# Performance work log

Hardware: AMD Instinct MI355X
Metric: run time of the kernel (lower is better)

## Reference

```python
import jax, jax.numpy as jnp
import numpy as np

C, G = 128, 2000          # num_cells, total_genes
CE, GE, H = 64, 64, 256   # cell_embed_dim, gene_embed_dim, hidden_dim
F = CE + GE + 3           # FCGNN input: ctrl val + cell_embed + gene_embed + shift + num_cells


def setup_inputs() -> dict:
    key = jax.random.key(0)
    ks = jax.random.split(key, 13)
    s = 0.02
    return {
        "ctrl": jax.random.uniform(ks[0], (C, G), dtype=jnp.float32),
        "shift_vec": jax.random.normal(ks[1], (G,), dtype=jnp.float32),
        "gene_indices": jnp.arange(G, dtype=jnp.int32),
        # CellEmbedding params
        "ce_w1": jax.random.normal(ks[2], (G, H), dtype=jnp.float32) * s,
        "ce_b1": jnp.zeros((H,), dtype=jnp.float32),
        "ce_w2": jax.random.normal(ks[3], (H, CE), dtype=jnp.float32) * s,
        "ce_b2": jnp.zeros((CE,), dtype=jnp.float32),
        # gene embedding table
        "gene_table": jax.random.normal(ks[4], (G, GE), dtype=jnp.float32) * s,
        # FCGNN params
        "g_w1": jax.random.normal(ks[5], (F, H), dtype=jnp.float32) * s,
        "g_b1": jnp.zeros((H,), dtype=jnp.float32),
        "g_w2": jax.random.normal(ks[6], (2 * H, H), dtype=jnp.float32) * s,
        "g_b2": jnp.zeros((H,), dtype=jnp.float32),
        "g_w3": jax.random.normal(ks[7], (2 * H, 1), dtype=jnp.float32) * s,
        "g_b3": jnp.zeros((1,), dtype=jnp.float32),
    }


def reference(ctrl, shift_vec, gene_indices, ce_w1, ce_b1, ce_w2, ce_b2,
              gene_table, g_w1, g_b1, g_w2, g_b2, g_w3, g_b3):
    num_cells = ctrl.shape[0]
    num_genes = gene_indices.shape[0]

    # CellEmbedding: fc2(elu(fc1(ctrl)))  -> [C, CE]
    ce = jax.nn.elu(ctrl @ ce_w1 + ce_b1) @ ce_w2 + ce_b2

    ctrl_g = ctrl[:, gene_indices]           # [C, Gn]
    shift = shift_vec[gene_indices]          # [Gn]
    ge = gene_table[gene_indices]            # [Gn, GE]

    # Build [C, Gn, F] feature tensor (ctrl val, cell embed, gene embed, shift, num_cells)
    z = jnp.concatenate([
        ctrl_g[:, :, None],
        jnp.broadcast_to(ce[:, None, :], (num_cells, num_genes, ce.shape[1])),
        jnp.broadcast_to(ge[None, :, :], (num_cells, num_genes, ge.shape[1])),
        jnp.broadcast_to(shift[None, :, None], (num_cells, num_genes, 1)),
        jnp.full((num_cells, num_genes, 1), float(num_cells), dtype=ctrl.dtype),
    ], axis=2)

    # FCGNN applied per gene (vectorized over gene axis); pooling is mean over cells (axis 0)
    x = jax.nn.elu(z @ g_w1 + g_b1)                                   # [C, Gn, H]
    p = x.mean(axis=0)                                                # [Gn, H]
    x = jnp.concatenate([x, jnp.broadcast_to(p[None], x.shape)], -1) @ g_w2 + g_b2
    p = x.mean(axis=0)
    x = jax.nn.elu(jnp.concatenate([x, jnp.broadcast_to(p[None], x.shape)], -1)) @ g_w3 + g_b3
    out = x[..., 0]                                                   # [C, Gn]

    # softmax over cells (torch Softmax(dim=0) after transpose/squeeze)
    return jax.nn.softmax(out, axis=0)
```

## Files before the change

### kernel.cpp

```cpp
#include <hip/hip_runtime.h>
#include <math.h>

#define G_GENES 2000
#define C_CELLS 128
#define H_DIM   256
#define CE_DIM  64
#define LDAe    260

typedef __attribute__((ext_vector_type(8))) short short8;
typedef __attribute__((ext_vector_type(4))) float floatx4;

__device__ __forceinline__ float eluf(float x) {
    float e = __expf(x) - 1.0f;
    return x > 0.0f ? x : e;
}
__device__ __forceinline__ unsigned short f2bf(float v) {
    unsigned u = __float_as_uint(v);
    u += 0x7FFF + ((u >> 16) & 1);
    return (unsigned short)(u >> 16);
}

__global__ __launch_bounds__(1024) void k_prep(
    const float* __restrict__ ctrl, const float* __restrict__ ce_w1,
    const float* __restrict__ ce_b1, const float* __restrict__ ce_w2,
    const float* __restrict__ ce_b2, const float* __restrict__ g_w1,
    const float* __restrict__ g_b1, const float* __restrict__ shiftv,
    const int* __restrict__ gidx, const float* __restrict__ gtab,
    const float* __restrict__ g_w2,
    float* __restrict__ Atc, unsigned short* __restrict__ w2abt,
    float* __restrict__ Bvg)
{
    const int b = blockIdx.x;
    const int t = threadIdx.x;

    if (b < C_CELLS) {
        __shared__ float crow[G_GENES];
        __shared__ float hidp[4][H_DIM];
        __shared__ float hid[H_DIM];
        __shared__ float celp[16 * CE_DIM];
        __shared__ float cel[CE_DIM];
        const int c = b;
        for (int i = t; i < G_GENES; i += 1024) crow[i] = ctrl[(size_t)c * G_GENES + i];
        __syncthreads();

        {
            const int h = t & 255, kq = t >> 8;
            float s[10];
            #pragma unroll
            for (int j = 0; j < 10; ++j) s[j] = 0.f;
            const float* w = ce_w1 + (size_t)(kq * 500) * H_DIM + h;
            const float* cr = crow + kq * 500;
            for (int k0 = 0; k0 < 50; ++k0) {
                #pragma unroll
                for (int j = 0; j < 10; ++j)
                    s[j] = fmaf(cr[k0 * 10 + j], w[(size_t)(k0 * 10 + j) * H_DIM], s[j]);
            }
            float ss = 0.f;
            #pragma unroll
            for (int j = 0; j < 10; ++j) ss += s[j];
            hidp[kq][h] = ss;
        }
        __syncthreads();
        if (t < H_DIM)
            hid[t] = eluf(hidp[0][t] + hidp[1][t] + hidp[2][t] + hidp[3][t] + ce_b1[t]);
        __syncthreads();

        {
            const int e = t & 63, grp = t >> 6;
            float cp = 0.f;
            #pragma unroll
            for (int hh = 0; hh < 16; ++hh)
                cp = fmaf(hid[grp * 16 + hh], ce_w2[(size_t)(grp * 16 + hh) * CE_DIM + e], cp);
            celp[grp * CE_DIM + e] = cp;
        }
        __syncthreads();
        if (t < CE_DIM) {
            float s = ce_b2[t];
            #pragma unroll
            for (int grp = 0; grp < 16; ++grp) s += celp[grp * CE_DIM + t];
            cel[t] = s;
        }
        __syncthreads();
        if (t < H_DIM) {
            float a = 0.f;
            #pragma unroll 8
            for (int e = 0; e < CE_DIM; ++e) a = fmaf(cel[e], g_w1[(size_t)(1 + e) * H_DIM + t], a);
            Atc[(size_t)c * H_DIM + t] = a;
        }
    } else if (b < C_CELLS + 8) {
        const int n  = (b - C_CELLS) * 32 + (t >> 5);
        const int k0 = (t & 31) * 8;
        unsigned v[8];
        #pragma unroll
        for (int j = 0; j < 8; ++j) v[j] = f2bf(g_w2[(size_t)(k0 + j) * H_DIM + n]);
        uint4 pk;
        pk.x = v[0] | (v[1] << 16);
        pk.y = v[2] | (v[3] << 16);
        pk.z = v[4] | (v[5] << 16);
        pk.w = v[6] | (v[7] << 16);
        *(uint4*)&w2abt[(size_t)n * H_DIM + k0] = pk;
    } else {
        const int g = (b - C_CELLS - 8) * 4 + (t >> 8);
        const int h = t & 255;
        const int idx = gidx[g];
        float bv = g_b1[h] + 128.0f * g_w1[(size_t)130 * H_DIM + h]
                 + shiftv[idx] * g_w1[(size_t)129 * H_DIM + h];
        #pragma unroll 8
        for (int e = 0; e < CE_DIM; ++e)
            bv = fmaf(gtab[(size_t)idx * CE_DIM + e], g_w1[(size_t)(65 + e) * H_DIM + h], bv);
        Bvg[(size_t)g * H_DIM + h] = bv;
    }
}

__global__ __launch_bounds__(512, 4) void k_main(
    const float* __restrict__ ctrl, const int* __restrict__ gidx,
    const float* __restrict__ g_w1, const float* __restrict__ g_w2,
    const float* __restrict__ g_b2, const float* __restrict__ g_w3,
    const float* __restrict__ Atc, const float* __restrict__ Bvg,
    const unsigned short* __restrict__ w2abt, float* __restrict__ out)
{
    __shared__ __align__(16) unsigned short x1t[C_CELLS * LDAe];
    __shared__ __align__(16) float scratch[8 * LDAe];
    __shared__ __align__(16) float Bvl[H_DIM];
    __shared__ __align__(16) float w1l[H_DIM];
    __shared__ float qv[H_DIM];
    __shared__ float w3v[H_DIM];
    __shared__ float cc[C_CELLS];
    __shared__ float wred[4];

    const int g = blockIdx.x;
    const int t = threadIdx.x;
    const int idx = gidx[g];

    const int lane = t & 63;
    const int w    = t >> 6;
    const int quad = lane >> 4;
    const int nlo  = lane & 15;
    const int wm   = w >> 2;
    const int wn   = w & 3;

    const unsigned short* bbase = w2abt + (size_t)(wn * 64 + nlo) * H_DIM + quad * 8;
    short8 bcur[4];
    #pragma unroll
    for (int nt = 0; nt < 4; ++nt)
        bcur[nt] = *(const short8*)(bbase + (size_t)nt * 16 * H_DIM);

    if (t < C_CELLS) cc[t] = ctrl[(size_t)t * G_GENES + idx];
    if (t < H_DIM) {
        Bvl[t] = Bvg[(size_t)g * H_DIM + t];
        w1l[t] = g_w1[t];
        w3v[t] = g_w3[t];
    }
    __syncthreads();

    {
        const int ho = t & 31, cgrp = t >> 5;
        const int h0 = ho * 8;
        float4 wv0 = *(const float4*)(w1l + h0);
        float4 wv1 = *(const float4*)(w1l + h0 + 4);
        float4 bv0 = *(const float4*)(Bvl + h0);
        float4 bv1 = *(const float4*)(Bvl + h0 + 4);
        float s[8];
        #pragma unroll
        for (int j = 0; j < 8; ++j) s[j] = 0.f;
        #pragma unroll
        for (int i = 0; i < 8; ++i) {
            const int c = cgrp * 8 + i;
            const float ccv = cc[c];
            float4 a0 = *(const float4*)(Atc + (size_t)c * H_DIM + h0);
            float4 a1 = *(const float4*)(Atc + (size_t)c * H_DIM + h0 + 4);
            float v0 = eluf(fmaf(ccv, wv0.x, a0.x + bv0.x));
            float v1 = eluf(fmaf(ccv, wv0.y, a0.y + bv0.y));
            float v2 = eluf(fmaf(ccv, wv0.z, a0.z + bv0.z));
            float v3 = eluf(fmaf(ccv, wv0.w, a0.w + bv0.w));
            float v4 = eluf(fmaf(ccv, wv1.x, a1.x + bv1.x));
            float v5 = eluf(fmaf(ccv, wv1.y, a1.y + bv1.y));
            float v6 = eluf(fmaf(ccv, wv1.z, a1.z + bv1.z));
            float v7 = eluf(fmaf(ccv, wv1.w, a1.w + bv1.w));
            s[0] += v0; s[1] += v1; s[2] += v2; s[3] += v3;
            s[4] += v4; s[5] += v5; s[6] += v6; s[7] += v7;
            uint4 pk;
            pk.x = (unsigned)f2bf(v0) | ((unsigned)f2bf(v1) << 16);
            pk.y = (unsigned)f2bf(v2) | ((unsigned)f2bf(v3) << 16);
            pk.z = (unsigned)f2bf(v4) | ((unsigned)f2bf(v5) << 16);
            pk.w = (unsigned)f2bf(v6) | ((unsigned)f2bf(v7) << 16);
            *(uint4*)&x1t[c * LDAe + h0] = pk;
        }
        #pragma unroll
        for (int j = 0; j < 8; ++j) s[j] += __shfl_xor(s[j], 32);
        if (lane < 32) {
            float4 p0 = {s[0], s[1], s[2], s[3]};
            float4 p1 = {s[4], s[5], s[6], s[7]};
            *(float4*)&scratch[w * LDAe + h0] = p0;
            *(float4*)&scratch[w * LDAe + h0 + 4] = p1;
        }
    }
    __syncthreads();

    floatx4 acc[4][4];
    #pragma unroll
    for (int mt = 0; mt < 4; ++mt)
        #pragma unroll
        for (int nt = 0; nt < 4; ++nt)
            acc[mt][nt] = (floatx4){0.f, 0.f, 0.f, 0.f};

    const unsigned short* abase = &x1t[(wm * 64 + nlo) * LDAe + quad * 8];

    #pragma unroll
    for (int kt = 0; kt < 8; ++kt) {
        short8 af[4];
        #pragma unroll
        for (int mt = 0; mt < 4; ++mt)
            af[mt] = *(const short8*)(abase + mt * 16 * LDAe + kt * 32);
        short8 bnx[4];
        if (kt < 7) {
            #pragma unroll
            for (int nt = 0; nt < 4; ++nt)
                bnx[nt] = *(const short8*)(bbase + (size_t)nt * 16 * H_DIM + (kt + 1) * 32);
        }
        #pragma unroll
        for (int nt = 0; nt < 4; ++nt)
            #pragma unroll
            for (int mt = 0; mt < 4; ++mt)
                acc[mt][nt] = __builtin_amdgcn_mfma_f32_16x16x32_bf16(af[mt], bcur[nt], acc[mt][nt], 0, 0, 0);
        if (kt < 7) {
            #pragma unroll
            for (int nt = 0; nt < 4; ++nt) bcur[nt] = bnx[nt];
        }
    }

    if (t < H_DIM) {
        float ps = 0.f;
        #pragma unroll
        for (int w2 = 0; w2 < 8; ++w2) ps += scratch[w2 * LDAe + t];
        w1l[t] = ps * (1.0f / 128.0f);
    }
    __syncthreads();

    {
        const int j = t & 255, hf = t >> 8;
        float qp = 0.f;
        const float* w2b = g_w2 + (size_t)(H_DIM + hf * 128) * H_DIM + j;
        const float* pv = w1l + hf * 128;
        #pragma unroll 16
        for (int h = 0; h < 128; ++h) qp = fmaf(pv[h], w2b[(size_t)h * H_DIM], qp);
        if (hf) Bvl[j] = qp;
        __syncthreads();
        if (!hf) qv[j] = qp + Bvl[j] + g_b2[j];
    }
    __syncthreads();

    float* red2 = scratch;
    float qj[4], w3j[4];
    #pragma unroll
    for (int nt = 0; nt < 4; ++nt) {
        const int j = wn * 64 + nt * 16 + nlo;
        qj[nt] = qv[j];
        w3j[nt] = w3v[j];
    }
    #pragma unroll
    for (int mt = 0; mt < 4; ++mt) {
        #pragma unroll
        for (int reg = 0; reg < 4; ++reg) {
            float part = 0.f;
            #pragma unroll
            for (int nt = 0; nt < 4; ++nt)
                part = fmaf(eluf(acc[mt][nt][reg] + qj[nt]), w3j[nt], part);
            part += __shfl_xor(part, 1);
            part += __shfl_xor(part, 2);
            part += __shfl_xor(part, 4);
            part += __shfl_xor(part, 8);
            if (nlo == 0)
                red2[(wm * 64 + mt * 16 + quad * 4 + reg) * 5 + wn] = part;
        }
    }
    __syncthreads();

    float s = 0.f, e = 0.f;
    if (t < C_CELLS) {
        s = red2[t * 5 + 0] + red2[t * 5 + 1] + red2[t * 5 + 2] + red2[t * 5 + 3];
        float m = s;
        #pragma unroll
        for (int off = 1; off < 64; off <<= 1) m = fmaxf(m, __shfl_xor(m, off));
        if (lane == 0) wred[w] = m;
    }
    __syncthreads();
    if (t < C_CELLS) {
        const float m = fmaxf(wred[0], wred[1]);
        e = __expf(s - m);
        float S = e;
        #pragma unroll
        for (int off = 1; off < 64; off <<= 1) S += __shfl_xor(S, off);
        if (lane == 0) wred[2 + w] = S;
    }
    __syncthreads();
    if (t < C_CELLS) out[(size_t)t * G_GENES + g] = e / (wred[2] + wred[3]);
}

extern "C" void kernel_launch(void* const* d_in, const int* in_sizes, int n_in,
                              void* d_out, int out_size, void* d_ws, size_t ws_size,
                              hipStream_t stream) {
    const float* ctrl   = (const float*)d_in[0];
    const float* shiftv = (const float*)d_in[1];
    const int*   gidx   = (const int*)d_in[2];
    const float* ce_w1  = (const float*)d_in[3];
    const float* ce_b1  = (const float*)d_in[4];
    const float* ce_w2  = (const float*)d_in[5];
    const float* ce_b2  = (const float*)d_in[6];
    const float* gtab   = (const float*)d_in[7];
    const float* g_w1   = (const float*)d_in[8];
    const float* g_b1   = (const float*)d_in[9];
    const float* g_w2   = (const float*)d_in[10];
    const float* g_b2   = (const float*)d_in[11];
    const float* g_w3   = (const float*)d_in[12];

    char* ws = (char*)d_ws;
    float* Atc            = (float*)(ws);
    unsigned short* w2abt = (unsigned short*)(ws + 128 * 1024);
    float* Bvg            = (float*)(ws + 256 * 1024);
    float* out            = (float*)d_out;

    k_prep<<<C_CELLS + 8 + G_GENES / 4, 1024, 0, stream>>>(
        ctrl, ce_w1, ce_b1, ce_w2, ce_b2, g_w1, g_b1, shiftv, gidx, gtab, g_w2,
        Atc, w2abt, Bvg);
    k_main<<<G_GENES, 512, 0, stream>>>(ctrl, gidx, g_w1, g_w2, g_b2, g_w3,
                                        Atc, Bvg, w2abt, out);
}
```

Measured before the change: 217.9 us.

## Hoist per-gene pooled-mean projection into a batched kernel; pair cells in prep

Adds a new kernel, k_pq, that computes the layer-1 mean over cells and its projection through the pooled half of g_w2 for 8 genes per block. Each g_w2 read is reused across genes instead of being re-read by every gene block. k_main then loads the precomputed q vector, which drops its fp32 sum reduction, the matvec and two barriers. The cell-embedding prep now handles two cells per block, so each ce_w1 load serves two rows. The trade-offs are an extra launch, layer-1 activations (ELU) being computed twice, and an intermediate q_all buffer written to and read back from global memory.

```diff
diff --git a/kernel.cpp b/kernel.cpp
--- a/kernel.cpp
+++ b/kernel.cpp
@@ -33,62 +33,75 @@
     const int b = blockIdx.x;
     const int t = threadIdx.x;
 
-    if (b < C_CELLS) {
-        __shared__ float crow[G_GENES];
-        __shared__ float hidp[4][H_DIM];
-        __shared__ float hid[H_DIM];
-        __shared__ float celp[16 * CE_DIM];
-        __shared__ float cel[CE_DIM];
-        const int c = b;
-        for (int i = t; i < G_GENES; i += 1024) crow[i] = ctrl[(size_t)c * G_GENES + i];
+    if (b < 64) {
+        __shared__ float crow[2][G_GENES];
+        __shared__ float hidp[4][2][H_DIM];
+        __shared__ float hid[2][H_DIM];
+        __shared__ float celp[16][2][CE_DIM];
+        __shared__ float cel[2][CE_DIM];
+        const int c0 = b * 2;
+        for (int i = t; i < G_GENES; i += 1024) {
+            crow[0][i] = ctrl[(size_t)c0 * G_GENES + i];
+            crow[1][i] = ctrl[(size_t)(c0 + 1) * G_GENES + i];
+        }
         __syncthreads();
 
         {
             const int h = t & 255, kq = t >> 8;
-            float s[10];
-            #pragma unroll
-            for (int j = 0; j < 10; ++j) s[j] = 0.f;
+            float a0 = 0.f, a1 = 0.f, b0 = 0.f, b1 = 0.f;
             const float* w = ce_w1 + (size_t)(kq * 500) * H_DIM + h;
-            const float* cr = crow + kq * 500;
-            for (int k0 = 0; k0 < 50; ++k0) {
-                #pragma unroll
-                for (int j = 0; j < 10; ++j)
-                    s[j] = fmaf(cr[k0 * 10 + j], w[(size_t)(k0 * 10 + j) * H_DIM], s[j]);
+            const float* r0 = crow[0] + kq * 500;
+            const float* r1 = crow[1] + kq * 500;
+            #pragma unroll 5
+            for (int k = 0; k < 500; k += 2) {
+                float w0 = w[(size_t)k * H_DIM];
+                float w1v = w[(size_t)(k + 1) * H_DIM];
+                a0 = fmaf(r0[k], w0, a0);     b0 = fmaf(r1[k], w0, b0);
+                a1 = fmaf(r0[k + 1], w1v, a1); b1 = fmaf(r1[k + 1], w1v, b1);
             }
-            float ss = 0.f;
-            #pragma unroll
-            for (int j = 0; j < 10; ++j) ss += s[j];
-            hidp[kq][h] = ss;
-        }
-        __syncthreads();
-        if (t < H_DIM)
-            hid[t] = eluf(hidp[0][t] + hidp[1][t] + hidp[2][t] + hidp[3][t] + ce_b1[t]);
+            hidp[kq][0][h] = a0 + a1;
+            hidp[kq][1][h] = b0 + b1;
+        }
+        __syncthreads();
+        if (t < 512) {
+            const int cc_ = t >> 8, h = t & 255;
+            hid[cc_][h] = eluf(hidp[0][cc_][h] + hidp[1][cc_][h] + hidp[2][cc_][h]
+                             + hidp[3][cc_][h] + ce_b1[h]);
+        }
         __syncthreads();
 
         {
             const int e = t & 63, grp = t >> 6;
-            float cp = 0.f;
-            #pragma unroll
-            for (int hh = 0; hh < 16; ++hh)
-                cp = fmaf(hid[grp * 16 + hh], ce_w2[(size_t)(grp * 16 + hh) * CE_DIM + e], cp);
-            celp[grp * CE_DIM + e] = cp;
-        }
-        __syncthreads();
-        if (t < CE_DIM) {
-            float s = ce_b2[t];
-            #pragma unroll
-            for (int grp = 0; grp < 16; ++grp) s += celp[grp * CE_DIM + t];
-            cel[t] = s;
-        }
-        __syncthreads();
-        if (t < H_DIM) {
+            float c0p = 0.f, c1p = 0.f;
+            #pragma unroll
+            for (int hh = 0; hh < 16; ++hh) {
+                const int h = grp * 16 + hh;
+                float wv = ce_w2[(size_t)h * CE_DIM + e];
+                c0p = fmaf(hid[0][h], wv, c0p);
+                c1p = fmaf(hid[1][h], wv, c1p);
+            }
+            celp[grp][0][e] = c0p;
+            celp[grp][1][e] = c1p;
+        }
+        __syncthreads();
+        if (t < 128) {
+            const int cc_ = t >> 6, e = t & 63;
+            float s = ce_b2[e];
+            #pragma unroll
+            for (int grp = 0; grp < 16; ++grp) s += celp[grp][cc_][e];
+            cel[cc_][e] = s;
+        }
+        __syncthreads();
+        if (t < 512) {
+            const int cc_ = t >> 8, h = t & 255;
             float a = 0.f;
             #pragma unroll 8
-            for (int e = 0; e < CE_DIM; ++e) a = fmaf(cel[e], g_w1[(size_t)(1 + e) * H_DIM + t], a);
-            Atc[(size_t)c * H_DIM + t] = a;
-        }
-    } else if (b < C_CELLS + 8) {
-        const int n  = (b - C_CELLS) * 32 + (t >> 5);
+            for (int e = 0; e < CE_DIM; ++e)
+                a = fmaf(cel[cc_][e], g_w1[(size_t)(1 + e) * H_DIM + h], a);
+            Atc[(size_t)(c0 + cc_) * H_DIM + h] = a;
+        }
+    } else if (b < 72) {
+        const int n  = (b - 64) * 32 + (t >> 5);
         const int k0 = (t & 31) * 8;
         unsigned v[8];
         #pragma unroll
@@ -100,7 +113,7 @@
         pk.w = v[6] | (v[7] << 16);
         *(uint4*)&w2abt[(size_t)n * H_DIM + k0] = pk;
     } else {
-        const int g = (b - C_CELLS - 8) * 4 + (t >> 8);
+        const int g = (b - 72) * 4 + (t >> 8);
         const int h = t & 255;
         const int idx = gidx[g];
         float bv = g_b1[h] + 128.0f * g_w1[(size_t)130 * H_DIM + h]
@@ -112,15 +125,83 @@
     }
 }
 
+__global__ __launch_bounds__(1024) void k_pq(
+    const float* __restrict__ ctrl, const int* __restrict__ gidx,
+    const float* __restrict__ g_w1, const float* __restrict__ g_w2,
+    const float* __restrict__ g_b2, const float* __restrict__ Atc,
+    const float* __restrict__ Bvg, float* __restrict__ q_all)
+{
+    __shared__ float ccl[C_CELLS][8];
+    __shared__ float pp[4][8][H_DIM];
+    __shared__ float pf[8][H_DIM];
+
+    const int g0 = blockIdx.x * 8;
+    const int t = threadIdx.x;
+
+    {
+        const int c = t >> 3, gg = t & 7;
+        if (t < 1024) ccl[c][gg] = ctrl[(size_t)c * G_GENES + gidx[g0 + gg]];
+    }
+    __syncthreads();
+
+    const int h = t & 255, cq = t >> 8;
+    {
+        const float w1h = g_w1[h];
+        float bv[8];
+        #pragma unroll
+        for (int gg = 0; gg < 8; ++gg) bv[gg] = Bvg[(size_t)(g0 + gg) * H_DIM + h];
+        float s[8];
+        #pragma unroll
+        for (int gg = 0; gg < 8; ++gg) s[gg] = 0.f;
+        for (int ci = 0; ci < 32; ++ci) {
+            const int c = cq * 32 + ci;
+            const float at = Atc[(size_t)c * H_DIM + h];
+            #pragma unroll
+            for (int gg = 0; gg < 8; ++gg)
+                s[gg] += eluf(fmaf(ccl[c][gg], w1h, at + bv[gg]));
+        }
+        #pragma unroll
+        for (int gg = 0; gg < 8; ++gg) pp[cq][gg][h] = s[gg];
+    }
+    __syncthreads();
+
+    {
+        const int i = t, gg = i >> 7, hh2 = (i & 127) * 2;
+        #pragma unroll
+        for (int u = 0; u < 2; ++u) {
+            const int hh = hh2 + u;
+            pf[gg][hh] = (pp[0][gg][hh] + pp[1][gg][hh] + pp[2][gg][hh] + pp[3][gg][hh])
+                         * (1.0f / 128.0f);
+        }
+    }
+    __syncthreads();
+
+    {
+        const int j = t & 255, gp = t >> 8;
+        float q0 = g_b2[j], q1 = g_b2[j];
+        const float* w2b = g_w2 + (size_t)H_DIM * H_DIM + j;
+        const float* p0 = pf[gp * 2];
+        const float* p1 = pf[gp * 2 + 1];
+        #pragma unroll 8
+        for (int hh = 0; hh < H_DIM; ++hh) {
+            const float wv = w2b[(size_t)hh * H_DIM];
+            q0 = fmaf(p0[hh], wv, q0);
+            q1 = fmaf(p1[hh], wv, q1);
+        }
+        q_all[(size_t)(g0 + gp * 2) * H_DIM + j] = q0;
+        q_all[(size_t)(g0 + gp * 2 + 1) * H_DIM + j] = q1;
+    }
+}
+
 __global__ __launch_bounds__(512, 4) void k_main(
     const float* __restrict__ ctrl, const int* __restrict__ gidx,
-    const float* __restrict__ g_w1, const float* __restrict__ g_w2,
-    const float* __restrict__ g_b2, const float* __restrict__ g_w3,
+    const float* __restrict__ g_w1, const float* __restrict__ g_w3,
     const float* __restrict__ Atc, const float* __restrict__ Bvg,
-    const unsigned short* __restrict__ w2abt, float* __restrict__ out)
+    const float* __restrict__ q_all, const unsigned short* __restrict__ w2abt,
+    float* __restrict__ out)
 {
     __shared__ __align__(16) unsigned short x1t[C_CELLS * LDAe];
-    __shared__ __align__(16) float scratch[8 * LDAe];
+    __shared__ float red2[C_CELLS * 5];
     __shared__ __align__(16) float Bvl[H_DIM];
     __shared__ __align__(16) float w1l[H_DIM];
     __shared__ float qv[H_DIM];
@@ -149,6 +230,7 @@
     if (t < H_DIM) {
         Bvl[t] = Bvg[(size_t)g * H_DIM + t];
         w1l[t] = g_w1[t];
+        qv[t]  = q_all[(size_t)g * H_DIM + t];
         w3v[t] = g_w3[t];
     }
     __syncthreads();
@@ -160,9 +242,6 @@
         float4 wv1 = *(const float4*)(w1l + h0 + 4);
         float4 bv0 = *(const float4*)(Bvl + h0);
         float4 bv1 = *(const float4*)(Bvl + h0 + 4);
-        float s[8];
-        #pragma unroll
-        for (int j = 0; j < 8; ++j) s[j] = 0.f;
         #pragma unroll
         for (int i = 0; i < 8; ++i) {
             const int c = cgrp * 8 + i;
@@ -177,8 +256,6 @@
             float v5 = eluf(fmaf(ccv, wv1.y, a1.y + bv1.y));
             float v6 = eluf(fmaf(ccv, wv1.z, a1.z + bv1.z));
             float v7 = eluf(fmaf(ccv, wv1.w, a1.w + bv1.w));
-            s[0] += v0; s[1] += v1; s[2] += v2; s[3] += v3;
-            s[4] += v4; s[5] += v5; s[6] += v6; s[7] += v7;
             uint4 pk;
             pk.x = (unsigned)f2bf(v0) | ((unsigned)f2bf(v1) << 16);
             pk.y = (unsigned)f2bf(v2) | ((unsigned)f2bf(v3) << 16);
@@ -186,14 +263,6 @@
             pk.w = (unsigned)f2bf(v6) | ((unsigned)f2bf(v7) << 16);
             *(uint4*)&x1t[c * LDAe + h0] = pk;
         }
-        #pragma unroll
-        for (int j = 0; j < 8; ++j) s[j] += __shfl_xor(s[j], 32);
-        if (lane < 32) {
-            float4 p0 = {s[0], s[1], s[2], s[3]};
-            float4 p1 = {s[4], s[5], s[6], s[7]};
-            *(float4*)&scratch[w * LDAe + h0] = p0;
-            *(float4*)&scratch[w * LDAe + h0 + 4] = p1;
-        }
     }
     __syncthreads();
 
@@ -229,28 +298,6 @@
         }
     }
 
-    if (t < H_DIM) {
-        float ps = 0.f;
-        #pragma unroll
-        for (int w2 = 0; w2 < 8; ++w2) ps += scratch[w2 * LDAe + t];
-        w1l[t] = ps * (1.0f / 128.0f);
-    }
-    __syncthreads();
-
-    {
-        const int j = t & 255, hf = t >> 8;
-        float qp = 0.f;
-        const float* w2b = g_w2 + (size_t)(H_DIM + hf * 128) * H_DIM + j;
-        const float* pv = w1l + hf * 128;
-        #pragma unroll 16
-        for (int h = 0; h < 128; ++h) qp = fmaf(pv[h], w2b[(size_t)h * H_DIM], qp);
-        if (hf) Bvl[j] = qp;
-        __syncthreads();
-        if (!hf) qv[j] = qp + Bvl[j] + g_b2[j];
-    }
-    __syncthreads();
-
-    float* red2 = scratch;
     float qj[4], w3j[4];
     #pragma unroll
     for (int nt = 0; nt < 4; ++nt) {
@@ -318,11 +365,12 @@
     float* Atc            = (float*)(ws);
     unsigned short* w2abt = (unsigned short*)(ws + 128 * 1024);
     float* Bvg            = (float*)(ws + 256 * 1024);
+    float* q_all          = (float*)(ws + 256 * 1024 + (size_t)G_GENES * H_DIM * 4);
     float* out            = (float*)d_out;
 
-    k_prep<<<C_CELLS + 8 + G_GENES / 4, 1024, 0, stream>>>(
+    k_prep<<<64 + 8 + G_GENES / 4, 1024, 0, stream>>>(
         ctrl, ce_w1, ce_b1, ce_w2, ce_b2, g_w1, g_b1, shiftv, gidx, gtab, g_w2,
         Atc, w2abt, Bvg);
-    k_main<<<G_GENES, 512, 0, stream>>>(ctrl, gidx, g_w1, g_w2, g_b2, g_w3,
-                                        Atc, Bvg, w2abt, out);
-}
+    k_pq<<<G_GENES / 8, 1024, 0, stream>>>(ctrl, gidx, g_w1, g_w2, g_b2, Atc, Bvg, q_all);
+    k_main<<<G_GENES, 512, 0, stream>>>(ctrl, gidx, g_w1, g_w3, Atc, Bvg, q_all, w2abt, out);
+}
```

New measurement: 238.7 us. 9.6% more time.

## Split-K the cell embedding matmul across many blocks and precompute bf16 transposed w2 halves

Applied to the files above, without the earlier changes.

The cell embedding fc1 is restructured from 128 big blocks into 1024 split-K blocks that write partial sums, followed by a small finishing kernel that reduces them and computes the rest of the embedding. The pooled-term matvec in the main kernel now reads a bf16 transposed copy of the second half of g_w2 instead of strided fp32 loads. Atc loads are hoisted ahead of the first barrier in the main kernel, and the bf16 packing now uses the library conversion. The split-K path adds an extra launch and a global partial-sum buffer. The bf16 weights reduce precision in the pooled term.

```diff
diff --git a/kernel.cpp b/kernel.cpp
--- a/kernel.cpp
+++ b/kernel.cpp
@@ -1,4 +1,5 @@
 #include <hip/hip_runtime.h>
+#include <hip/hip_bf16.h>
 #include <math.h>
 
 #define G_GENES 2000
@@ -14,93 +15,68 @@
     float e = __expf(x) - 1.0f;
     return x > 0.0f ? x : e;
 }
-__device__ __forceinline__ unsigned short f2bf(float v) {
-    unsigned u = __float_as_uint(v);
-    u += 0x7FFF + ((u >> 16) & 1);
-    return (unsigned short)(u >> 16);
-}
-
-__global__ __launch_bounds__(1024) void k_prep(
+__device__ __forceinline__ unsigned pk2(float a, float b) {
+    __hip_bfloat162 h2 = __float22bfloat162_rn(make_float2(a, b));
+    unsigned r; __builtin_memcpy(&r, &h2, 4); return r;
+}
+union U8 { unsigned u[4]; short8 s; uint4 v; };
+
+__global__ __launch_bounds__(512) void k_g1(
     const float* __restrict__ ctrl, const float* __restrict__ ce_w1,
-    const float* __restrict__ ce_b1, const float* __restrict__ ce_w2,
-    const float* __restrict__ ce_b2, const float* __restrict__ g_w1,
-    const float* __restrict__ g_b1, const float* __restrict__ shiftv,
-    const int* __restrict__ gidx, const float* __restrict__ gtab,
-    const float* __restrict__ g_w2,
-    float* __restrict__ Atc, unsigned short* __restrict__ w2abt,
-    float* __restrict__ Bvg)
+    const float* __restrict__ g_w1, const float* __restrict__ g_b1,
+    const float* __restrict__ shiftv, const int* __restrict__ gidx,
+    const float* __restrict__ gtab, const float* __restrict__ g_w2,
+    float* __restrict__ hidpart, unsigned short* __restrict__ w2abt,
+    unsigned short* __restrict__ w2bbt, float* __restrict__ Bvg)
 {
     const int b = blockIdx.x;
     const int t = threadIdx.x;
 
-    if (b < C_CELLS) {
-        __shared__ float crow[G_GENES];
-        __shared__ float hidp[4][H_DIM];
-        __shared__ float hid[H_DIM];
-        __shared__ float celp[16 * CE_DIM];
-        __shared__ float cel[CE_DIM];
-        const int c = b;
-        for (int i = t; i < G_GENES; i += 1024) crow[i] = ctrl[(size_t)c * G_GENES + i];
+    if (b < 1024) {
+        __shared__ float crow[2][128];
+        const int cpair = b >> 4;
+        const int kc    = b & 15;
+        const int csub  = t >> 8;
+        const int h     = t & 255;
+        const int c     = cpair * 2 + csub;
+
+        if (h < 125) crow[csub][h] = ctrl[(size_t)c * G_GENES + kc * 125 + h];
         __syncthreads();
 
-        {
-            const int h = t & 255, kq = t >> 8;
-            float s[10];
-            #pragma unroll
-            for (int j = 0; j < 10; ++j) s[j] = 0.f;
-            const float* w = ce_w1 + (size_t)(kq * 500) * H_DIM + h;
-            const float* cr = crow + kq * 500;
-            for (int k0 = 0; k0 < 50; ++k0) {
-                #pragma unroll
-                for (int j = 0; j < 10; ++j)
-                    s[j] = fmaf(cr[k0 * 10 + j], w[(size_t)(k0 * 10 + j) * H_DIM], s[j]);
-            }
-            float ss = 0.f;
-            #pragma unroll
-            for (int j = 0; j < 10; ++j) ss += s[j];
-            hidp[kq][h] = ss;
-        }
-        __syncthreads();
-        if (t < H_DIM)
-            hid[t] = eluf(hidp[0][t] + hidp[1][t] + hidp[2][t] + hidp[3][t] + ce_b1[t]);
-        __syncthreads();
-
-        {
-            const int e = t & 63, grp = t >> 6;
-            float cp = 0.f;
-            #pragma unroll
-            for (int hh = 0; hh < 16; ++hh)
-                cp = fmaf(hid[grp * 16 + hh], ce_w2[(size_t)(grp * 16 + hh) * CE_DIM + e], cp);
-            celp[grp * CE_DIM + e] = cp;
-        }
-        __syncthreads();
-        if (t < CE_DIM) {
-            float s = ce_b2[t];
-            #pragma unroll
-            for (int grp = 0; grp < 16; ++grp) s += celp[grp * CE_DIM + t];
-            cel[t] = s;
-        }
-        __syncthreads();
-        if (t < H_DIM) {
-            float a = 0.f;
-            #pragma unroll 8
-            for (int e = 0; e < CE_DIM; ++e) a = fmaf(cel[e], g_w1[(size_t)(1 + e) * H_DIM + t], a);
-            Atc[(size_t)c * H_DIM + t] = a;
-        }
-    } else if (b < C_CELLS + 8) {
-        const int n  = (b - C_CELLS) * 32 + (t >> 5);
+        float s0 = 0.f, s1 = 0.f, s2 = 0.f, s3 = 0.f, s4 = 0.f;
+        const float* w = ce_w1 + (size_t)(kc * 125) * H_DIM + h;
+        const float* cr = crow[csub];
+        #pragma unroll 5
+        for (int k = 0; k < 125; k += 5) {
+            s0 = fmaf(cr[k + 0], w[(size_t)(k + 0) * H_DIM], s0);
+            s1 = fmaf(cr[k + 1], w[(size_t)(k + 1) * H_DIM], s1);
+            s2 = fmaf(cr[k + 2], w[(size_t)(k + 2) * H_DIM], s2);
+            s3 = fmaf(cr[k + 3], w[(size_t)(k + 3) * H_DIM], s3);
+            s4 = fmaf(cr[k + 4], w[(size_t)(k + 4) * H_DIM], s4);
+        }
+        hidpart[((size_t)kc * C_CELLS + c) * H_DIM + h] = ((s0 + s1) + (s2 + s3)) + s4;
+    } else if (b < 1040) {
+        const int n  = (b - 1024) * 16 + (t >> 5);
         const int k0 = (t & 31) * 8;
-        unsigned v[8];
-        #pragma unroll
-        for (int j = 0; j < 8; ++j) v[j] = f2bf(g_w2[(size_t)(k0 + j) * H_DIM + n]);
-        uint4 pk;
-        pk.x = v[0] | (v[1] << 16);
-        pk.y = v[2] | (v[3] << 16);
-        pk.z = v[4] | (v[5] << 16);
-        pk.w = v[6] | (v[7] << 16);
-        *(uint4*)&w2abt[(size_t)n * H_DIM + k0] = pk;
+        float v[8];
+        #pragma unroll
+        for (int j = 0; j < 8; ++j) v[j] = g_w2[(size_t)(k0 + j) * H_DIM + n];
+        U8 u;
+        u.u[0] = pk2(v[0], v[1]); u.u[1] = pk2(v[2], v[3]);
+        u.u[2] = pk2(v[4], v[5]); u.u[3] = pk2(v[6], v[7]);
+        *(uint4*)&w2abt[(size_t)n * H_DIM + k0] = u.v;
+    } else if (b < 1056) {
+        const int j  = (b - 1040) * 16 + (t >> 5);
+        const int h0 = (t & 31) * 8;
+        float v[8];
+        #pragma unroll
+        for (int u2 = 0; u2 < 8; ++u2) v[u2] = g_w2[(size_t)(H_DIM + h0 + u2) * H_DIM + j];
+        U8 u;
+        u.u[0] = pk2(v[0], v[1]); u.u[1] = pk2(v[2], v[3]);
+        u.u[2] = pk2(v[4], v[5]); u.u[3] = pk2(v[6], v[7]);
+        *(uint4*)&w2bbt[(size_t)j * H_DIM + h0] = u.v;
     } else {
-        const int g = (b - C_CELLS - 8) * 4 + (t >> 8);
+        const int g = (b - 1056) * 2 + (t >> 8);
         const int h = t & 255;
         const int idx = gidx[g];
         float bv = g_b1[h] + 128.0f * g_w1[(size_t)130 * H_DIM + h]
@@ -112,15 +88,52 @@
     }
 }
 
+__global__ __launch_bounds__(256) void k_fin(
+    const float* __restrict__ hidpart, const float* __restrict__ ce_b1,
+    const float* __restrict__ ce_w2, const float* __restrict__ ce_b2,
+    const float* __restrict__ g_w1, float* __restrict__ Atc)
+{
+    __shared__ float hid[H_DIM];
+    __shared__ float celp[4 * CE_DIM];
+    __shared__ float cel[CE_DIM];
+    const int c = blockIdx.x;
+    const int t = threadIdx.x;
+
+    float s = ce_b1[t];
+    #pragma unroll
+    for (int kc = 0; kc < 16; ++kc)
+        s += hidpart[((size_t)kc * C_CELLS + c) * H_DIM + t];
+    hid[t] = eluf(s);
+    __syncthreads();
+
+    {
+        const int e = t & 63, q4 = t >> 6;
+        float cp = 0.f;
+        #pragma unroll 8
+        for (int hh = 0; hh < 64; ++hh)
+            cp = fmaf(hid[q4 * 64 + hh], ce_w2[(size_t)(q4 * 64 + hh) * CE_DIM + e], cp);
+        celp[q4 * CE_DIM + e] = cp;
+    }
+    __syncthreads();
+    if (t < CE_DIM)
+        cel[t] = ce_b2[t] + celp[t] + celp[CE_DIM + t] + celp[2 * CE_DIM + t] + celp[3 * CE_DIM + t];
+    __syncthreads();
+
+    float a = 0.f;
+    #pragma unroll 8
+    for (int e = 0; e < CE_DIM; ++e) a = fmaf(cel[e], g_w1[(size_t)(1 + e) * H_DIM + t], a);
+    Atc[(size_t)c * H_DIM + t] = a;
+}
+
 __global__ __launch_bounds__(512, 4) void k_main(
     const float* __restrict__ ctrl, const int* __restrict__ gidx,
-    const float* __restrict__ g_w1, const float* __restrict__ g_w2,
-    const float* __restrict__ g_b2, const float* __restrict__ g_w3,
-    const float* __restrict__ Atc, const float* __restrict__ Bvg,
-    const unsigned short* __restrict__ w2abt, float* __restrict__ out)
+    const float* __restrict__ g_w1, const float* __restrict__ g_b2,
+    const float* __restrict__ g_w3, const float* __restrict__ Atc,
+    const float* __restrict__ Bvg, const unsigned short* __restrict__ w2abt,
+    const unsigned short* __restrict__ w2bbt, float* __restrict__ out)
 {
     __shared__ __align__(16) unsigned short x1t[C_CELLS * LDAe];
-    __shared__ __align__(16) float scratch[8 * LDAe];
+    __shared__ __align__(16) float scratch[8 * 258];
     __shared__ __align__(16) float Bvl[H_DIM];
     __shared__ __align__(16) float w1l[H_DIM];
     __shared__ float qv[H_DIM];
@@ -139,6 +152,15 @@
     const int wm   = w >> 2;
     const int wn   = w & 3;
 
+    const int ho = t & 31, cgrp = t >> 5;
+    const int h0 = ho * 8;
+    float4 A0[8], A1[8];
+    #pragma unroll
+    for (int i = 0; i < 8; ++i) {
+        const int c = cgrp * 8 + i;
+        A0[i] = *(const float4*)(Atc + (size_t)c * H_DIM + h0);
+        A1[i] = *(const float4*)(Atc + (size_t)c * H_DIM + h0 + 4);
+    }
     const unsigned short* bbase = w2abt + (size_t)(wn * 64 + nlo) * H_DIM + quad * 8;
     short8 bcur[4];
     #pragma unroll
@@ -154,8 +176,6 @@
     __syncthreads();
 
     {
-        const int ho = t & 31, cgrp = t >> 5;
-        const int h0 = ho * 8;
         float4 wv0 = *(const float4*)(w1l + h0);
         float4 wv1 = *(const float4*)(w1l + h0 + 4);
         float4 bv0 = *(const float4*)(Bvl + h0);
@@ -167,23 +187,19 @@
         for (int i = 0; i < 8; ++i) {
             const int c = cgrp * 8 + i;
             const float ccv = cc[c];
-            float4 a0 = *(const float4*)(Atc + (size_t)c * H_DIM + h0);
-            float4 a1 = *(const float4*)(Atc + (size_t)c * H_DIM + h0 + 4);
-            float v0 = eluf(fmaf(ccv, wv0.x, a0.x + bv0.x));
-            float v1 = eluf(fmaf(ccv, wv0.y, a0.y + bv0.y));
-            float v2 = eluf(fmaf(ccv, wv0.z, a0.z + bv0.z));
-            float v3 = eluf(fmaf(ccv, wv0.w, a0.w + bv0.w));
-            float v4 = eluf(fmaf(ccv, wv1.x, a1.x + bv1.x));
-            float v5 = eluf(fmaf(ccv, wv1.y, a1.y + bv1.y));
-            float v6 = eluf(fmaf(ccv, wv1.z, a1.z + bv1.z));
-            float v7 = eluf(fmaf(ccv, wv1.w, a1.w + bv1.w));
+            float v0 = eluf(fmaf(ccv, wv0.x, A0[i].x + bv0.x));
+            float v1 = eluf(fmaf(ccv, wv0.y, A0[i].y + bv0.y));
+            float v2 = eluf(fmaf(ccv, wv0.z, A0[i].z + bv0.z));
+            float v3 = eluf(fmaf(ccv, wv0.w, A0[i].w + bv0.w));
+            float v4 = eluf(fmaf(ccv, wv1.x, A1[i].x + bv1.x));
+            float v5 = eluf(fmaf(ccv, wv1.y, A1[i].y + bv1.y));
+            float v6 = eluf(fmaf(ccv, wv1.z, A1[i].z + bv1.z));
+            float v7 = eluf(fmaf(ccv, wv1.w, A1[i].w + bv1.w));
             s[0] += v0; s[1] += v1; s[2] += v2; s[3] += v3;
             s[4] += v4; s[5] += v5; s[6] += v6; s[7] += v7;
             uint4 pk;
-            pk.x = (unsigned)f2bf(v0) | ((unsigned)f2bf(v1) << 16);
-            pk.y = (unsigned)f2bf(v2) | ((unsigned)f2bf(v3) << 16);
-            pk.z = (unsigned)f2bf(v4) | ((unsigned)f2bf(v5) << 16);
-            pk.w = (unsigned)f2bf(v6) | ((unsigned)f2bf(v7) << 16);
+            pk.x = pk2(v0, v1); pk.y = pk2(v2, v3);
+            pk.z = pk2(v4, v5); pk.w = pk2(v6, v7);
             *(uint4*)&x1t[c * LDAe + h0] = pk;
         }
         #pragma unroll
@@ -191,8 +207,8 @@
         if (lane < 32) {
             float4 p0 = {s[0], s[1], s[2], s[3]};
             float4 p1 = {s[4], s[5], s[6], s[7]};
-            *(float4*)&scratch[w * LDAe + h0] = p0;
-            *(float4*)&scratch[w * LDAe + h0 + 4] = p1;
+            *(float4*)&scratch[w * 258 + h0] = p0;
+            *(float4*)&scratch[w * 258 + h0 + 4] = p1;
         }
     }
     __syncthreads();
@@ -232,7 +248,7 @@
     if (t < H_DIM) {
         float ps = 0.f;
         #pragma unroll
-        for (int w2 = 0; w2 < 8; ++w2) ps += scratch[w2 * LDAe + t];
+        for (int w2 = 0; w2 < 8; ++w2) ps += scratch[w2 * 258 + t];
         w1l[t] = ps * (1.0f / 128.0f);
     }
     __syncthreads();
@@ -240,10 +256,17 @@
     {
         const int j = t & 255, hf = t >> 8;
         float qp = 0.f;
-        const float* w2b = g_w2 + (size_t)(H_DIM + hf * 128) * H_DIM + j;
+        const unsigned* wrow = (const unsigned*)(w2bbt + (size_t)j * H_DIM + hf * 128);
         const float* pv = w1l + hf * 128;
-        #pragma unroll 16
-        for (int h = 0; h < 128; ++h) qp = fmaf(pv[h], w2b[(size_t)h * H_DIM], qp);
+        #pragma unroll 8
+        for (int d = 0; d < 64; ++d) {
+            const unsigned u = wrow[d];
+            const float wlo = __uint_as_float(u << 16);
+            const float whi = __uint_as_float(u & 0xffff0000u);
+            const float2 a = *(const float2*)&pv[2 * d];
+            qp = fmaf(a.x, wlo, qp);
+            qp = fmaf(a.y, whi, qp);
+        }
         if (hf) Bvl[j] = qp;
         __syncthreads();
         if (!hf) qv[j] = qp + Bvl[j] + g_b2[j];
@@ -317,12 +340,14 @@
     char* ws = (char*)d_ws;
     float* Atc            = (float*)(ws);
     unsigned short* w2abt = (unsigned short*)(ws + 128 * 1024);
-    float* Bvg            = (float*)(ws + 256 * 1024);
+    unsigned short* w2bbt = (unsigned short*)(ws + 256 * 1024);
+    float* Bvg            = (float*)(ws + 384 * 1024);
+    float* hidpart        = (float*)(ws + 384 * 1024 + (size_t)G_GENES * H_DIM * 4);
     float* out            = (float*)d_out;
 
-    k_prep<<<C_CELLS + 8 + G_GENES / 4, 1024, 0, stream>>>(
-        ctrl, ce_w1, ce_b1, ce_w2, ce_b2, g_w1, g_b1, shiftv, gidx, gtab, g_w2,
-        Atc, w2abt, Bvg);
-    k_main<<<G_GENES, 512, 0, stream>>>(ctrl, gidx, g_w1, g_w2, g_b2, g_w3,
-                                        Atc, Bvg, w2abt, out);
-}
+    k_g1<<<2056, 512, 0, stream>>>(
+        ctrl, ce_w1, g_w1, g_b1, shiftv, gidx, gtab, g_w2, hidpart, w2abt, w2bbt, Bvg);
+    k_fin<<<C_CELLS, 256, 0, stream>>>(hidpart, ce_b1, ce_w2, ce_b2, g_w1, Atc);
+    k_main<<<G_GENES, 512, 0, stream>>>(ctrl, gidx, g_w1, g_b2, g_w3,
+                                        Atc, Bvg, w2abt, w2bbt, out);
+}
```

Measured after the change: 228.6 us. 4.9% more time.
